# Optimization experiments

Hardware: AMD Instinct MI355X
Metric: run time of the kernel (lower is better)

Reference implementation:

```python
import jax, jax.numpy as jnp
import numpy as np

B, T, X, E, H, L = 4096, 32, 256, 32, 512, 2  # batch, theta_size, x_size, n_masks, hidden, num_hidden_layers


def _prelu(v, a):
    # PReLU with per-channel slope a (broadcast [E,H] or [B,E,H] vs [B,E,H])
    return jnp.where(v >= 0, v, a * v)


def setup_inputs() -> dict:
    key = jax.random.key(0)
    ks = jax.random.split(key, 12)
    theta = jax.random.normal(ks[0], (B, T), dtype=jnp.float32)
    x = jax.random.normal(ks[1], (B, X), dtype=jnp.float32)
    masks = jax.random.randint(ks[2], (E, T), 0, 2, dtype=jnp.int32)
    masks = masks.at[:, 0].set(1)  # guarantee non-empty subsets
    D = T + X
    s_in = 1.0 / np.sqrt(D)
    s_h = 1.0 / np.sqrt(H)
    # first Linear, split into theta-part and x-part of the weight matrix
    W1t = jax.random.normal(ks[3], (E, T, H), dtype=jnp.float32) * s_in
    W1x = jax.random.normal(ks[4], (E, X, H), dtype=jnp.float32) * s_in
    b1 = jax.random.normal(ks[5], (E, H), dtype=jnp.float32) * s_in
    a1 = jnp.full((E, H), 0.25, dtype=jnp.float32)  # PReLU init
    # num_layers hidden Linear(H,H) + PReLU
    Wh = jax.random.normal(ks[6], (L, E, H, H), dtype=jnp.float32) * s_h
    bh = jax.random.normal(ks[7], (L, E, H), dtype=jnp.float32) * s_h
    ah = jnp.full((L, E, H), 0.25, dtype=jnp.float32)
    # output Linear(H, 1) -> squeeze(-1)
    Wo = jax.random.normal(ks[8], (E, H), dtype=jnp.float32) * s_h
    bo = jax.random.normal(ks[9], (E,), dtype=jnp.float32) * s_h
    return {"theta": theta, "x": x, "masks": masks, "W1t": W1t, "W1x": W1x,
            "b1": b1, "a1": a1, "Wh": Wh, "bh": bh, "ah": ah, "Wo": Wo, "bo": bo}


def reference(theta, x, masks, W1t, W1x, b1, a1, Wh, bh, ah, Wo, bo):
    # theta[..., mask] followed by Linear is equivalent to masking theta per
    # expert and contracting with the full per-expert theta weight block.
    m = masks.astype(theta.dtype)                      # [E, T]
    tm = theta[:, None, :] * m[None, :, :]             # [B, E, T]
    h = (jnp.einsum('bet,eth->beh', tm, W1t)
         + jnp.einsum('bx,exh->beh', x, W1x) + b1)     # [B, E, H]
    h = _prelu(h, a1)
    for i in range(Wh.shape[0]):                       # small fixed layer loop
        h = jnp.einsum('beh,ehk->bek', h, Wh[i]) + bh[i]
        h = _prelu(h, ah[i])
    # Linear(H,1).squeeze(-1), stacked over masks on the last dim -> [B, E]
    return jnp.einsum('beh,eh->be', h, Wo) + bo
```

## Files before the change

kernel.cpp:

```cpp
#include <hip/hip_runtime.h>
#include <stdint.h>
#include <type_traits>

#define B_SZ 4096
#define T_SZ 32
#define X_SZ 256
#define E_SZ 32
#define H_SZ 512
#define BM   128
#define AROW 1040

typedef __attribute__((ext_vector_type(8))) short  short8;
typedef __attribute__((ext_vector_type(4))) float  floatx4;

__device__ __forceinline__ unsigned pk2(float a, float b) {
  unsigned r;
  asm("v_cvt_pk_bf16_f32 %0, %1, %2" : "=v"(r) : "v"(a), "v"(b));
  return r;
}

__global__ __launch_bounds__(256) void prep_kernel(
    const float* __restrict__ W1t, const float* __restrict__ W1x,
    const int* __restrict__ masks, const float* __restrict__ Wh,
    uint4* __restrict__ wcat, uint4* __restrict__ whf) {
  __shared__ unsigned lds[16 * 516];
  const int c = blockIdx.x;
  const int t = threadIdx.x;

  const float* base;
  bool needMask = false;
  int e1 = 0;
  if (c >= 288) {
    int cc = c - 288;
    int le = cc >> 4, kt = cc & 15;
    base = Wh + ((size_t)le * H_SZ + kt * 32) * H_SZ;
  } else {
    int e = c / 9, kt = c - e * 9;
    e1 = e;
    if (kt == 0) { base = W1t + (size_t)e * T_SZ * H_SZ; needMask = true; }
    else          base = W1x + ((size_t)e * X_SZ + (kt - 1) * 32) * H_SZ;
  }

#pragma unroll
  for (int i = 0; i < 8; ++i) {
    int g  = i * 256 + t;
    int k2 = g >> 7, np = g & 127;
    const float* r0 = base + (size_t)(2 * k2) * H_SZ + np * 4;
    float4 a = *(const float4*)r0;
    float4 b = *(const float4*)(r0 + H_SZ);
    if (needMask) {
      float s0 = (float)masks[e1 * T_SZ + 2 * k2];
      float s1 = (float)masks[e1 * T_SZ + 2 * k2 + 1];
      a.x *= s0; a.y *= s0; a.z *= s0; a.w *= s0;
      b.x *= s1; b.y *= s1; b.z *= s1; b.w *= s1;
    }
    *(uint4*)&lds[k2 * 516 + np * 4] =
        make_uint4(pk2(a.x, b.x), pk2(a.y, b.y), pk2(a.z, b.z), pk2(a.w, b.w));
  }
  __syncthreads();

  uint4* outp = (c < 288) ? (wcat + (size_t)c * 2048)
                          : (whf + (size_t)(c - 288) * 2048);
  const int w = t >> 6, l = t & 63, q = l >> 4, l16 = l & 15;
#pragma unroll
  for (int j = 0; j < 8; ++j) {
    int nb = w * 8 + j;
    int n  = nb * 16 + l16;
    int kb = 4 * q;
    uint4 v;
    v.x = lds[(kb + 0) * 516 + n];
    v.y = lds[(kb + 1) * 516 + n];
    v.z = lds[(kb + 2) * 516 + n];
    v.w = lds[(kb + 3) * 516 + n];
    outp[nb * 64 + l] = v;
  }
}

__global__ __launch_bounds__(512, 2) void mlp_kernel(
    const float* __restrict__ theta, const float* __restrict__ x,
    const short8* __restrict__ wcat, const short8* __restrict__ whf,
    const float* __restrict__ b1, const float* __restrict__ a1,
    const float* __restrict__ bh, const float* __restrict__ ah,
    const float* __restrict__ Wo, const float* __restrict__ bo,
    float* __restrict__ out) {
  __shared__ __align__(16) char smA[BM * AROW];
  const int tid = threadIdx.x;
  const int bid = blockIdx.x;
  const int xcd = bid & 7;
  const int t8  = bid >> 3;
  const int e   = xcd * 4 + (t8 >> 5);
  const int m0  = (t8 & 31) * BM;
  const int w   = tid >> 6, l = tid & 63, l16 = l & 15, quad = l >> 4;

  {
    int r = tid >> 2, c = tid & 3;
    const float* tp = theta + (size_t)(m0 + r) * T_SZ + c * 8;
    float4 t0 = *(const float4*)tp;
    float4 t1 = *(const float4*)(tp + 4);
    *(uint4*)(smA + r * AROW + c * 16) =
        make_uint4(pk2(t0.x, t0.y), pk2(t0.z, t0.w), pk2(t1.x, t1.y), pk2(t1.z, t1.w));
    const float* xp = x + (size_t)(m0 + r) * X_SZ + c * 64;
#pragma unroll
    for (int j = 0; j < 8; ++j) {
      float4 a = *(const float4*)(xp + j * 8);
      float4 b = *(const float4*)(xp + j * 8 + 4);
      *(uint4*)(smA + r * AROW + 64 + c * 128 + j * 16) =
          make_uint4(pk2(a.x, a.y), pk2(a.z, a.w), pk2(b.x, b.y), pk2(b.z, b.w));
    }
  }
  __syncthreads();

  floatx4 acc[8][4];
  const int u0 = w * 256 + l;
  const char* ar0 = smA + l16 * AROW + quad * 16;
  const char* ar1 = ar0 + 4 * 16 * AROW;

  auto gemm = [&](const short8* wbase, auto nktc) {
    constexpr int NKT = decltype(nktc)::value;
#pragma unroll
    for (int mb = 0; mb < 8; ++mb)
#pragma unroll
      for (int i = 0; i < 4; ++i) acc[mb][i] = (floatx4)(0.f);
    const short8* wu = wbase;
    short8 bA[4], bB[4];
#pragma unroll
    for (int i = 0; i < 4; ++i) bA[i] = wu[u0 + i * 64];
#pragma unroll
    for (int kt = 0; kt < NKT; ++kt) {
      if (kt + 1 < NKT) {
        const short8* wn = wu + 2048;
        if (kt & 1) {
#pragma unroll
          for (int i = 0; i < 4; ++i) bA[i] = wn[u0 + i * 64];
        } else {
#pragma unroll
          for (int i = 0; i < 4; ++i) bB[i] = wn[u0 + i * 64];
        }
      }
      short8 af[8];
#pragma unroll
      for (int mb = 0; mb < 4; ++mb)
        af[mb] = *(const short8*)(ar0 + mb * (16 * AROW) + kt * 64);
#pragma unroll
      for (int mb = 0; mb < 4; ++mb)
        af[mb + 4] = *(const short8*)(ar1 + mb * (16 * AROW) + kt * 64);
#pragma unroll
      for (int mb = 0; mb < 8; ++mb)
#pragma unroll
        for (int i = 0; i < 4; ++i)
          acc[mb][i] = __builtin_amdgcn_mfma_f32_16x16x32_bf16(
              af[mb], (kt & 1) ? bB[i] : bA[i], acc[mb][i], 0, 0, 0);
      wu += 2048;
    }
  };

  auto epi_store = [&](const float* bias, const float* slope) {
    float bb[4], aa[4];
#pragma unroll
    for (int i = 0; i < 4; ++i) {
      int col = w * 64 + i * 16 + l16;
      bb[i] = bias[col];
      aa[i] = slope[col];
    }
    __syncthreads();
#pragma unroll
    for (int mb = 0; mb < 8; ++mb) {
#pragma unroll
      for (int i = 0; i < 4; ++i) {
        unsigned dw[4];
#pragma unroll
        for (int r = 0; r < 4; ++r) {
          float v = acc[mb][i][r] + bb[i];
          v = v >= 0.f ? v : aa[i] * v;
          float o  = __shfl_xor(v, 1, 64);
          float lo = (l16 & 1) ? o : v;
          float hi = (l16 & 1) ? v : o;
          dw[r] = pk2(lo, hi);
        }
        int col2  = w * 64 + i * 16 + (l16 & ~1);
        int rbase = (l16 & 1) * 2;
#pragma unroll
        for (int rr = 0; rr < 2; ++rr) {
          int row = mb * 16 + quad * 4 + rbase + rr;
          *(unsigned*)(smA + row * AROW + col2 * 2) = dw[rbase + rr];
        }
      }
    }
    __syncthreads();
  };

  gemm(wcat + (size_t)e * 9 * 2048, std::integral_constant<int, 9>{});
  epi_store(b1 + (size_t)e * H_SZ, a1 + (size_t)e * H_SZ);
  gemm(whf + (size_t)e * 16 * 2048, std::integral_constant<int, 16>{});
  epi_store(bh + (size_t)e * H_SZ, ah + (size_t)e * H_SZ);
  gemm(whf + (size_t)(E_SZ + e) * 16 * 2048, std::integral_constant<int, 16>{});
  {
    float bb[4], aa[4], wo[4];
#pragma unroll
    for (int i = 0; i < 4; ++i) {
      int col = w * 64 + i * 16 + l16;
      bb[i] = bh[(size_t)(E_SZ + e) * H_SZ + col];
      aa[i] = ah[(size_t)(E_SZ + e) * H_SZ + col];
      wo[i] = Wo[(size_t)e * H_SZ + col];
    }
    float ps[8][4];
#pragma unroll
    for (int mb = 0; mb < 8; ++mb)
#pragma unroll
      for (int r = 0; r < 4; ++r) ps[mb][r] = 0.f;
#pragma unroll
    for (int mb = 0; mb < 8; ++mb)
#pragma unroll
      for (int i = 0; i < 4; ++i)
#pragma unroll
        for (int r = 0; r < 4; ++r) {
          float v = acc[mb][i][r] + bb[i];
          v = v >= 0.f ? v : aa[i] * v;
          ps[mb][r] += v * wo[i];
        }
#pragma unroll
    for (int d = 1; d < 16; d <<= 1)
#pragma unroll
      for (int mb = 0; mb < 8; ++mb)
#pragma unroll
        for (int r = 0; r < 4; ++r) ps[mb][r] += __shfl_xor(ps[mb][r], d, 64);
    __syncthreads();
    float* scratch = (float*)smA;
    if (l16 == 0) {
#pragma unroll
      for (int mb = 0; mb < 8; ++mb)
#pragma unroll
        for (int r = 0; r < 4; ++r)
          scratch[(mb * 16 + quad * 4 + r) * 8 + w] = ps[mb][r];
    }
    __syncthreads();
    if (tid < BM) {
      float s = 0.f;
#pragma unroll
      for (int ww = 0; ww < 8; ++ww) s += scratch[tid * 8 + ww];
      out[(size_t)(m0 + tid) * E_SZ + e] = s + bo[e];
    }
  }
}

extern "C" void kernel_launch(void* const* d_in, const int* in_sizes, int n_in,
                              void* d_out, int out_size, void* d_ws, size_t ws_size,
                              hipStream_t stream) {
  const float* theta = (const float*)d_in[0];
  const float* x     = (const float*)d_in[1];
  const int*   masks = (const int*)d_in[2];
  const float* W1t   = (const float*)d_in[3];
  const float* W1x   = (const float*)d_in[4];
  const float* b1    = (const float*)d_in[5];
  const float* a1    = (const float*)d_in[6];
  const float* Wh    = (const float*)d_in[7];
  const float* bh    = (const float*)d_in[8];
  const float* ah    = (const float*)d_in[9];
  const float* Wo    = (const float*)d_in[10];
  const float* bo    = (const float*)d_in[11];
  float* out = (float*)d_out;

  uint4* wcat = (uint4*)d_ws;
  uint4* whf  = (uint4*)((char*)d_ws + (size_t)E_SZ * 9 * 2048 * 16);

  prep_kernel<<<1312, 256, 0, stream>>>(W1t, W1x, masks, Wh, wcat, whf);
  mlp_kernel<<<1024, 512, 0, stream>>>(theta, x, (const short8*)wcat,
                                       (const short8*)whf, b1, a1, bh, ah, Wo, bo,
                                       out);
}
```

Before: 343.5 us.

## Use 1024-thread blocks and store activations in MFMA fragment order in LDS

Doubles the mlp block to 16 waves, so each wave computes 32 output columns instead of 64, which halves the accumulator registers per wave. The activation tile in LDS is rearranged from padded row-major into a lane-ordered fragment layout, so A-operand reads become contiguous 16-byte per-lane loads. The epilogue writes PReLU outputs straight into that fragment layout for the next layer, and the final cross-wave reduction now sums 16 partials. This aims for more latency hiding through higher occupancy, at the cost of each wave re-reading the whole A tile from LDS and more barrier participants.

```diff
diff --git a/kernel.cpp b/kernel.cpp
--- a/kernel.cpp
+++ b/kernel.cpp
@@ -8,7 +8,6 @@
 #define E_SZ 32
 #define H_SZ 512
 #define BM   128
-#define AROW 1040
 
 typedef __attribute__((ext_vector_type(8))) short  short8;
 typedef __attribute__((ext_vector_type(4))) float  floatx4;
@@ -76,14 +75,14 @@
   }
 }
 
-__global__ __launch_bounds__(512, 2) void mlp_kernel(
+__global__ __launch_bounds__(1024, 4) void mlp_kernel(
     const float* __restrict__ theta, const float* __restrict__ x,
     const short8* __restrict__ wcat, const short8* __restrict__ whf,
     const float* __restrict__ b1, const float* __restrict__ a1,
     const float* __restrict__ bh, const float* __restrict__ ah,
     const float* __restrict__ Wo, const float* __restrict__ bo,
     float* __restrict__ out) {
-  __shared__ __align__(16) char smA[BM * AROW];
+  __shared__ __align__(16) char smA[16 * 8 * 64 * 16];
   const int tid = threadIdx.x;
   const int bid = blockIdx.x;
   const int xcd = bid & 7;
@@ -92,73 +91,62 @@
   const int m0  = (t8 & 31) * BM;
   const int w   = tid >> 6, l = tid & 63, l16 = l & 15, quad = l >> 4;
 
-  {
-    int r = tid >> 2, c = tid & 3;
-    const float* tp = theta + (size_t)(m0 + r) * T_SZ + c * 8;
-    float4 t0 = *(const float4*)tp;
-    float4 t1 = *(const float4*)(tp + 4);
-    *(uint4*)(smA + r * AROW + c * 16) =
-        make_uint4(pk2(t0.x, t0.y), pk2(t0.z, t0.w), pk2(t1.x, t1.y), pk2(t1.z, t1.w));
-    const float* xp = x + (size_t)(m0 + r) * X_SZ + c * 64;
-#pragma unroll
-    for (int j = 0; j < 8; ++j) {
-      float4 a = *(const float4*)(xp + j * 8);
-      float4 b = *(const float4*)(xp + j * 8 + 4);
-      *(uint4*)(smA + r * AROW + 64 + c * 128 + j * 16) =
-          make_uint4(pk2(a.x, a.y), pk2(a.z, a.w), pk2(b.x, b.y), pk2(b.z, b.w));
-    }
+  for (int g = tid; g < 9 * 512; g += 1024) {
+    int lane = g & 63, mb = (g >> 6) & 7, kt = g >> 9;
+    int row  = m0 + mb * 16 + (lane & 15);
+    int ks   = (lane >> 4) * 8;
+    const float* src = (kt == 0)
+                           ? (theta + (size_t)row * T_SZ + ks)
+                           : (x + (size_t)row * X_SZ + (kt - 1) * 32 + ks);
+    float4 a = *(const float4*)src;
+    float4 b = *(const float4*)(src + 4);
+    *(uint4*)(smA + (size_t)g * 16) =
+        make_uint4(pk2(a.x, a.y), pk2(a.z, a.w), pk2(b.x, b.y), pk2(b.z, b.w));
   }
   __syncthreads();
 
-  floatx4 acc[8][4];
-  const int u0 = w * 256 + l;
-  const char* ar0 = smA + l16 * AROW + quad * 16;
-  const char* ar1 = ar0 + 4 * 16 * AROW;
+  floatx4 acc[8][2];
+  const int u0 = w * 128 + l;
 
   auto gemm = [&](const short8* wbase, auto nktc) {
     constexpr int NKT = decltype(nktc)::value;
 #pragma unroll
     for (int mb = 0; mb < 8; ++mb)
 #pragma unroll
-      for (int i = 0; i < 4; ++i) acc[mb][i] = (floatx4)(0.f);
+      for (int i = 0; i < 2; ++i) acc[mb][i] = (floatx4)(0.f);
+    short8 bA[2], bB[2];
+    bA[0] = wbase[u0];
+    bA[1] = wbase[u0 + 64];
     const short8* wu = wbase;
-    short8 bA[4], bB[4];
-#pragma unroll
-    for (int i = 0; i < 4; ++i) bA[i] = wu[u0 + i * 64];
 #pragma unroll
     for (int kt = 0; kt < NKT; ++kt) {
       if (kt + 1 < NKT) {
         const short8* wn = wu + 2048;
-        if (kt & 1) {
-#pragma unroll
-          for (int i = 0; i < 4; ++i) bA[i] = wn[u0 + i * 64];
-        } else {
-#pragma unroll
-          for (int i = 0; i < 4; ++i) bB[i] = wn[u0 + i * 64];
-        }
+        if (kt & 1) { bA[0] = wn[u0]; bA[1] = wn[u0 + 64]; }
+        else        { bB[0] = wn[u0]; bB[1] = wn[u0 + 64]; }
       }
-      short8 af[8];
-#pragma unroll
-      for (int mb = 0; mb < 4; ++mb)
-        af[mb] = *(const short8*)(ar0 + mb * (16 * AROW) + kt * 64);
-#pragma unroll
-      for (int mb = 0; mb < 4; ++mb)
-        af[mb + 4] = *(const short8*)(ar1 + mb * (16 * AROW) + kt * 64);
-#pragma unroll
-      for (int mb = 0; mb < 8; ++mb)
-#pragma unroll
-        for (int i = 0; i < 4; ++i)
-          acc[mb][i] = __builtin_amdgcn_mfma_f32_16x16x32_bf16(
-              af[mb], (kt & 1) ? bB[i] : bA[i], acc[mb][i], 0, 0, 0);
+#pragma unroll
+      for (int h = 0; h < 2; ++h) {
+        short8 af[4];
+#pragma unroll
+        for (int m = 0; m < 4; ++m)
+          af[m] = *(const short8*)(smA + ((kt * 8 + h * 4 + m) * 64 + l) * 16);
+#pragma unroll
+        for (int m = 0; m < 4; ++m)
+#pragma unroll
+          for (int i = 0; i < 2; ++i)
+            acc[h * 4 + m][i] = __builtin_amdgcn_mfma_f32_16x16x32_bf16(
+                af[m], (kt & 1) ? bB[i] : bA[i], acc[h * 4 + m][i], 0, 0, 0);
+      }
       wu += 2048;
     }
   };
 
   auto epi_store = [&](const float* bias, const float* slope) {
-    float bb[4], aa[4];
-#pragma unroll
-    for (int i = 0; i < 4; ++i) {
-      int col = w * 64 + i * 16 + l16;
+    float bb[2], aa[2];
+#pragma unroll
+    for (int i = 0; i < 2; ++i) {
+      int col = w * 32 + i * 16 + l16;
       bb[i] = bias[col];
       aa[i] = slope[col];
     }
@@ -166,7 +154,7 @@
 #pragma unroll
     for (int mb = 0; mb < 8; ++mb) {
 #pragma unroll
-      for (int i = 0; i < 4; ++i) {
+      for (int i = 0; i < 2; ++i) {
         unsigned dw[4];
 #pragma unroll
         for (int r = 0; r < 4; ++r) {
@@ -177,12 +165,12 @@
           float hi = (l16 & 1) ? v : o;
           dw[r] = pk2(lo, hi);
         }
-        int col2  = w * 64 + i * 16 + (l16 & ~1);
         int rbase = (l16 & 1) * 2;
+        char* ubase = smA + ((w * 8 + mb) * 64) * 16 + (l16 & 6) * 2;
 #pragma unroll
         for (int rr = 0; rr < 2; ++rr) {
-          int row = mb * 16 + quad * 4 + rbase + rr;
-          *(unsigned*)(smA + row * AROW + col2 * 2) = dw[rbase + rr];
+          int lane_p = quad * 4 + rbase + rr + (i * 2 + (l16 >> 3)) * 16;
+          *(unsigned*)(ubase + lane_p * 16) = dw[rbase + rr];
         }
       }
     }
@@ -195,10 +183,10 @@
   epi_store(bh + (size_t)e * H_SZ, ah + (size_t)e * H_SZ);
   gemm(whf + (size_t)(E_SZ + e) * 16 * 2048, std::integral_constant<int, 16>{});
   {
-    float bb[4], aa[4], wo[4];
-#pragma unroll
-    for (int i = 0; i < 4; ++i) {
-      int col = w * 64 + i * 16 + l16;
+    float bb[2], aa[2], wo[2];
+#pragma unroll
+    for (int i = 0; i < 2; ++i) {
+      int col = w * 32 + i * 16 + l16;
       bb[i] = bh[(size_t)(E_SZ + e) * H_SZ + col];
       aa[i] = ah[(size_t)(E_SZ + e) * H_SZ + col];
       wo[i] = Wo[(size_t)e * H_SZ + col];
@@ -211,7 +199,7 @@
 #pragma unroll
     for (int mb = 0; mb < 8; ++mb)
 #pragma unroll
-      for (int i = 0; i < 4; ++i)
+      for (int i = 0; i < 2; ++i)
 #pragma unroll
         for (int r = 0; r < 4; ++r) {
           float v = acc[mb][i][r] + bb[i];
@@ -231,13 +219,13 @@
       for (int mb = 0; mb < 8; ++mb)
 #pragma unroll
         for (int r = 0; r < 4; ++r)
-          scratch[(mb * 16 + quad * 4 + r) * 8 + w] = ps[mb][r];
+          scratch[(mb * 16 + quad * 4 + r) * 16 + w] = ps[mb][r];
     }
     __syncthreads();
     if (tid < BM) {
       float s = 0.f;
 #pragma unroll
-      for (int ww = 0; ww < 8; ++ww) s += scratch[tid * 8 + ww];
+      for (int ww = 0; ww < 16; ++ww) s += scratch[tid * 16 + ww];
       out[(size_t)(m0 + tid) * E_SZ + e] = s + bo[e];
     }
   }
@@ -264,7 +252,7 @@
   uint4* whf  = (uint4*)((char*)d_ws + (size_t)E_SZ * 9 * 2048 * 16);
 
   prep_kernel<<<1312, 256, 0, stream>>>(W1t, W1x, masks, Wh, wcat, whf);
-  mlp_kernel<<<1024, 512, 0, stream>>>(theta, x, (const short8*)wcat,
-                                       (const short8*)whf, b1, a1, bh, ah, Wo, bo,
-                                       out);
-}
+  mlp_kernel<<<1024, 1024, 0, stream>>>(theta, x, (const short8*)wcat,
+                                        (const short8*)whf, b1, a1, bh, ah, Wo,
+                                        bo, out);
+}
```

New measurement: 373.2 us. +8.6%, slower.
